# Kernel tuning notes

Measured on AMD Instinct MI355X. Metric: run time of the kernel, lower is better.

The kernel has to match this reference:

```python
import jax, jax.numpy as jnp
import numpy as np

B, S, V, D, G, H, L, K = 32, 256, 100000, 128, 128, 256, 32, 3
ALPHA = 0.5


def lstm_pass(x, mask, W, U, b, reverse):
    # x: (B,S,I), mask: (B,S) bool. PyTorch gate order i,f,g,o.
    Bh = x.shape[0]
    Hd = U.shape[0]
    h0 = jnp.zeros((Bh, Hd), x.dtype)
    c0 = jnp.zeros((Bh, Hd), x.dtype)

    def step(carry, inp):
        h, c = carry
        xt, mt = inp
        g = xt @ W + h @ U + b
        i, f, gg, o = jnp.split(g, 4, axis=-1)
        i = jax.nn.sigmoid(i)
        f = jax.nn.sigmoid(f)
        gg = jnp.tanh(gg)
        o = jax.nn.sigmoid(o)
        cn = f * c + i * gg
        hn = o * jnp.tanh(cn)
        m = mt[:, None]
        h = jnp.where(m, hn, h)
        c = jnp.where(m, cn, c)
        return (h, c), h * m.astype(h.dtype)

    _, hs = jax.lax.scan(step, (h0, c0), (x.transpose(1, 0, 2), mask.T), reverse=reverse)
    return hs.transpose(1, 0, 2)  # (B,S,Hd), zero at padded steps (like pad_packed)


def setup_inputs() -> dict:
    key = jax.random.key(0)
    ks = jax.random.split(key, 24)
    word_inputs = jax.random.randint(ks[0], (B, S), 0, V)
    lens = jnp.sort(jax.random.randint(ks[1], (B,), S // 2, S + 1))[::-1]
    mask = (jnp.arange(S)[None, :] < lens[:, None])
    idx_inputs = jax.random.randint(ks[2], (B, S), 0, V)
    char_inputs = jax.random.randint(ks[3], (B * S, 4), 0, 100)
    char_seq_lengths = jnp.ones((B * S,), jnp.int64 if jax.config.jax_enable_x64 else jnp.int32)
    char_seq_recover = jnp.arange(B * S)
    s = lambda k, sh, sc: jax.random.normal(k, sh, jnp.float32) * sc
    I = D + G
    inp = {
        'word_inputs': word_inputs,
        'word_seq_lengths': lens,
        'char_inputs': char_inputs,
        'char_seq_lengths': char_seq_lengths,
        'char_seq_recover': char_seq_recover,
        'mask': mask,
        'idx_inputs': idx_inputs,
        'word_embedding': s(ks[4], (V, D), 0.1),
        'label_embedding': s(ks[5], (L, D), 0.1),
        'sent_W': s(ks[6], (D, G), 1.0 / np.sqrt(D)),
        'sent_b': jnp.zeros((G,), jnp.float32),
        'conv_W': s(ks[7], (L, L, K), 1.0 / np.sqrt(L * K)),
        'conv_b': jnp.zeros((L,), jnp.float32),
        'lstm_Wf': s(ks[8], (I, 4 * H // 2), 1.0 / np.sqrt(I)),
        'lstm_Uf': s(ks[9], (H // 2, 4 * H // 2), 1.0 / np.sqrt(H // 2)),
        'lstm_bf': jnp.zeros((4 * H // 2,), jnp.float32),
        'lstm_Wb': s(ks[10], (I, 4 * H // 2), 1.0 / np.sqrt(I)),
        'lstm_Ub': s(ks[11], (H // 2, 4 * H // 2), 1.0 / np.sqrt(H // 2)),
        'lstm_bb': jnp.zeros((4 * H // 2,), jnp.float32),
        'tag_W': s(ks[12], (H, L), 1.0 / np.sqrt(H)),
        'tag_b': jnp.zeros((L,), jnp.float32),
        'mem_W': s(ks[13], (H, L), 1.0 / np.sqrt(H)),
        'mem_b': jnp.zeros((L,), jnp.float32),
        'mem_bank': s(ks[14], (V, H), 0.1),
    }
    return inp


def reference(word_inputs, word_seq_lengths, char_inputs, char_seq_lengths, char_seq_recover,
              mask, idx_inputs, word_embedding, label_embedding, sent_W, sent_b,
              conv_W, conv_b, lstm_Wf, lstm_Uf, lstm_bf, lstm_Wb, lstm_Ub, lstm_bb,
              tag_W, tag_b, mem_W, mem_b, mem_bank):
    maskf = mask.astype(jnp.float32)
    # ---- WordRep: embeddings + label cosine similarity ----
    we = word_embedding[word_inputs]  # (B,S,D) gather
    wn = we / (jnp.linalg.norm(we, axis=-1, keepdims=True) + 1e-8)
    ln = label_embedding / (jnp.linalg.norm(label_embedding, axis=-1, keepdims=True) + 1e-8)
    label_embs = jnp.einsum('bsd,ld->bsl', wn, ln)  # (B,S,L)
    # ---- SentenceRep (projection stand-in) + label attention pooling ----
    sent_hidden = jnp.tanh(we @ sent_W + sent_b)  # (B,S,G)
    lf = jax.lax.conv_general_dilated(
        label_embs.transpose(0, 2, 1), conv_W, (1,), [(K // 2, K // 2)],
        dimension_numbers=('NCH', 'OIH', 'NCH')) + conv_b[None, :, None]
    lf = jax.nn.relu(lf).transpose(0, 2, 1)  # (B,S,L)
    lm = lf.max(axis=-1)  # (B,S)
    # partial (masked) softmax, exactly as in the torch code
    e = jnp.exp(lm) * maskf
    attn = e / e.sum(axis=1, keepdims=True)
    sent_rep = jnp.einsum('bs,bsg->bg', attn, sent_hidden)[:, None, :]  # bmm
    sent_rep = jnp.broadcast_to(sent_rep, (B, S, G))  # repeat over seq
    # ---- BiLSTM over concat(word, sentence) ----
    wr = jnp.concatenate([we, sent_rep], axis=-1)  # (B,S,D+G)
    hf = lstm_pass(wr, mask, lstm_Wf, lstm_Uf, lstm_bf, False)
    hb = lstm_pass(wr, mask, lstm_Wb, lstm_Ub, lstm_bb, True)
    feat = jnp.concatenate([hf, hb], axis=-1)  # (B,S,H)
    outputs = feat @ tag_W + tag_b  # (B,S,L)
    # ---- MemoryBank: gather keyed by word id, zero padded positions ----
    doc_h = mem_bank[word_inputs] * maskf[..., None]  # (B,S,H) irregular gather
    doc_rep = doc_h @ mem_W + mem_b  # mem2tag
    # bank update (side effect in torch; computed functionally, not returned)
    new_bank = mem_bank.at[idx_inputs.reshape(-1)].set(
        (feat * maskf[..., None]).reshape(-1, H))
    del new_bank
    return outputs * (1.0 - ALPHA) + doc_rep * ALPHA
```

## Files before the change

### kernel.cpp

```cpp
#include <hip/hip_runtime.h>
#include <hip/hip_bf16.h>

#define BB 32
#define SS 256
#define DD 128
#define GG 128
#define NG 512
#define LL 32
#define LOG2E 1.4426950408889634f

typedef unsigned short u16;
typedef __attribute__((ext_vector_type(8))) short short8;
typedef __attribute__((ext_vector_type(4))) float f32x4;

__device__ __forceinline__ float bf2f(u16 u){ return __uint_as_float(((unsigned)u)<<16); }
__device__ __forceinline__ u16 f2bf(float f){
    unsigned x = __float_as_uint(f);
    unsigned r = x + 0x7fffu + ((x>>16)&1u);
    return (u16)(r>>16);
}
__device__ __forceinline__ float tanh_f(float x){ float e=__expf(2.0f*x); return 1.0f - 2.0f/(e+1.0f); }

__device__ __forceinline__ float exp2_f(float x){
#if __has_builtin(__builtin_amdgcn_exp2f)
    return __builtin_amdgcn_exp2f(x);
#elif __has_builtin(__builtin_amdgcn_expf)
    return __builtin_amdgcn_expf(x);
#else
    return __expf(x * 0.6931471805599453f);
#endif
}
__device__ __forceinline__ float rcp_f(float x){
#if __has_builtin(__builtin_amdgcn_rcpf)
    return __builtin_amdgcn_rcpf(x);
#else
    return 1.0f / x;
#endif
}

__global__ void kflag(const u16* __restrict__ w, int* __restrict__ flags){
    int t = threadIdx.x;
    u16 v = w[2*t];
    int e = (v>>7)&0xFF;
    __shared__ int red[256];
    red[t] = (e>=0x90)?1:0; __syncthreads();
    for (int off=128;off>0;off>>=1){ if(t<off) red[t]+=red[t+off]; __syncthreads(); }
    if (t==0) flags[0] = (red[0] >= 32) ? 1 : 0;
}

struct PJobs { const void* src[20]; int n[20]; int p0[20]; int p1[20]; int type[20]; };

__global__ void kprep(PJobs jb, const int* __restrict__ flags, float* __restrict__ can,
                      u16* __restrict__ WcatT, u16* __restrict__ tagWT, u16* __restrict__ memWT){
    int id = blockIdx.y;
    int i = blockIdx.x*256 + threadIdx.x;
    if (i >= jb.n[id]) return;
    int f = flags[0];
    const void* src = jb.src[id];
    int p0 = jb.p0[id];
    int ty = jb.type[id];
    if (ty == 0){
        float v = f ? ((const float*)src)[i] : bf2f(((const u16*)src)[i]);
        can[p0 + i] = v;
    } else if (ty == 1){
        int c = i>>7, k = i&127;
        float v = f ? ((const float*)src)[k*jb.p1[id] + c] : bf2f(((const u16*)src)[k*jb.p1[id] + c]);
        WcatT[(size_t)(p0 + c)*128 + k] = f2bf(v);
    } else {
        int l = i&31, k = i>>5;
        float v = f ? ((const float*)src)[k*32 + l] : bf2f(((const u16*)src)[k*32 + l]);
        (p0 ? memWT : tagWT)[l*256 + k] = f2bf(v);
    }
}

__global__ void k0_prep(const float* __restrict__ labc, u16* __restrict__ WcatT){
    int r = blockIdx.x, t = threadIdx.x;
    __shared__ float red[128];
    float v = labc[r*DD + t];
    red[t] = v*v; __syncthreads();
    for (int off=64; off>0; off>>=1){ if (t<off) red[t]+=red[t+off]; __syncthreads(); }
    float inv = 1.0f/(sqrtf(red[0]) + 1e-8f);
    WcatT[(size_t)(1152 + r)*128 + t] = f2bf(v*inv);
    WcatT[(size_t)(1184 + r)*128 + t] = 0;
}

__global__ void k1_token(const int* __restrict__ wid, const void* __restrict__ wemb,
                         const int* __restrict__ flags,
                         u16* __restrict__ weC, float* __restrict__ invn){
    int blk = blockIdx.x;
    int t = threadIdx.x;
    int idx = wid[blk];
    float wv = flags[0] ? ((const float*)wemb)[(size_t)idx*DD + t]
                        : bf2f(((const u16*)wemb)[(size_t)idx*DD + t]);
    int b = blk>>8, s = blk&255;
    int m = s*BB + b;
    weC[(size_t)m*DD + t] = f2bf(wv);
    float sq = wv*wv;
    #pragma unroll
    for (int mk=32; mk>0; mk>>=1) sq += __shfl_xor(sq, mk);
    __shared__ float red2[2];
    if ((t&63)==0) red2[t>>6] = sq;
    __syncthreads();
    if (t==0) invn[m] = 1.0f/(sqrtf(red2[0]+red2[1]) + 1e-8f);
}

__global__ __launch_bounds__(256) void kgemm(const u16* __restrict__ weC,
                      const u16* __restrict__ WcatT,
                      const float* __restrict__ invn, const float* __restrict__ sentBc,
                      float* __restrict__ gpre4, float* __restrict__ sent_h,
                      float* __restrict__ lab_e){
    int mt = blockIdx.x;
    int nb = blockIdx.y;
    int t = threadIdx.x;
    int w4 = t>>6, l = t&63, li = l&15, lg = l>>4;
    int mbase = mt*64 + w4*16;
    int n0 = nb*64;
    short8 af[4];
    #pragma unroll
    for (int ks=0;ks<4;ks++)
        af[ks] = *(const short8*)&weC[(size_t)(mbase + li)*128 + ks*32 + lg*8];
    f32x4 acc[4];
    #pragma unroll
    for (int nt=0;nt<4;nt++){
        short8 bf[4];
        #pragma unroll
        for (int ks=0;ks<4;ks++)
            bf[ks] = *(const short8*)&WcatT[(size_t)(n0 + nt*16 + li)*128 + ks*32 + lg*8];
        f32x4 a; a[0]=0.f; a[1]=0.f; a[2]=0.f; a[3]=0.f;
        #pragma unroll
        for (int ks=0;ks<4;ks++)
            a = __builtin_amdgcn_mfma_f32_16x16x32_bf16(af[ks], bf[ks], a, 0,0,0);
        acc[nt] = a;
    }
    int mrow = mbase + lg*4;
    #pragma unroll
    for (int nt=0;nt<4;nt++){
        int n = n0 + nt*16 + li;
        if (n < 1024){
            int dir = n>>9, n2 = n&511;
            int q = n2>>7, cc = n2&127, w5 = cc>>4, li5 = cc&15;
            float sc = (q==2) ? 2.0f*LOG2E : LOG2E;
            #pragma unroll
            for (int r=0;r<4;r++){
                int m = mrow + r;
                int b = m&31, s = m>>5;
                int bg = b>>2, rb = b&3;
                gpre4[((size_t)((dir*8+bg)*256 + s)*8 + w5)*256 + (rb*16 + li5)*4 + q] = acc[nt][r]*sc;
            }
        } else if (n < 1152){
            int c = n - 1024;
            float bb = sentBc[c];
            #pragma unroll
            for (int r=0;r<4;r++){
                int m = mrow + r;
                int b = m&31, s = m>>5;
                sent_h[((size_t)(b*256+s))*128 + c] = tanh_f(acc[nt][r] + bb);
            }
        } else if (n < 1184){
            int c = n - 1152;
            #pragma unroll
            for (int r=0;r<4;r++){
                int m = mrow + r;
                int b = m&31, s = m>>5;
                lab_e[((size_t)(b*256+s))*32 + c] = acc[nt][r] * invn[m];
            }
        }
    }
}

__global__ __launch_bounds__(256) void k2_conv(const float* __restrict__ lab_e,
                        const float* __restrict__ convWc, const float* __restrict__ convBc,
                        const int* __restrict__ lens, float* __restrict__ e_ws){
    int b = blockIdx.x, stile = blockIdx.y, t = threadIdx.x;
    int sl = t>>3, oq = t&7;
    int s = stile*32 + sl;
    __shared__ float le_s[34*33];
    __shared__ float wle[LL*LL*3];
    __shared__ float wb[LL];
    int s0 = stile*32;
    for (int i=t; i<34*32; i+=256){
        int row = i>>5, col = i&31;
        int sg = s0 - 1 + row;
        le_s[row*33 + col] = (sg>=0 && sg<SS) ? lab_e[(size_t)b*SS*LL + sg*LL + col] : 0.f;
    }
    for (int i=t; i<LL*LL*3; i+=256) wle[i] = convWc[i];
    if (t < LL) wb[t] = convBc[t];
    __syncthreads();
    float lm = 0.f;
    #pragma unroll
    for (int op=0; op<4; op++){
        int o = oq*4 + op;
        float a0 = wb[o], a1 = 0.f, a2 = 0.f;
        #pragma unroll
        for (int i=0;i<LL;i++){
            a0 = fmaf(le_s[(sl+0)*33+i], wle[o*96 + i*3    ], a0);
            a1 = fmaf(le_s[(sl+1)*33+i], wle[o*96 + i*3 + 1], a1);
            a2 = fmaf(le_s[(sl+2)*33+i], wle[o*96 + i*3 + 2], a2);
        }
        lm = fmaxf(lm, fmaxf(a0+a1+a2, 0.f));
    }
    #pragma unroll
    for (int mk=1; mk<8; mk<<=1) lm = fmaxf(lm, __shfl_xor(lm, mk));
    if (oq == 0) e_ws[b*SS + s] = (s < lens[b]) ? __expf(lm) : 0.f;
}

__global__ void k3a_attn(const float* __restrict__ e_ws, const float* __restrict__ sent_h,
                         float* __restrict__ sr){
    int b = blockIdx.x, t = threadIdx.x;
    __shared__ float es[SS], red[SS], srp[2][GG];
    float ev = e_ws[b*SS + t];
    es[t]=ev; red[t]=ev; __syncthreads();
    for (int off=128; off>0; off>>=1){ if (t<off) red[t]+=red[t+off]; __syncthreads(); }
    float inv = 1.0f/red[0];
    int col = t&127, sh = t>>7;
    float a0 = 0.f, a1 = 0.f;
    int sb = sh*128;
    for (int s2=sb; s2<sb+128; s2+=2){
        a0 = fmaf(es[s2],   sent_h[((size_t)b*SS + s2)*GG + col], a0);
        a1 = fmaf(es[s2+1], sent_h[((size_t)b*SS + s2+1)*GG + col], a1);
    }
    srp[sh][col] = a0+a1;
    __syncthreads();
    if (t < GG) sr[b*GG + t] = (srp[0][t]+srp[1][t])*inv;
}

__global__ void k3b_cpart(const float* __restrict__ sr,
                          const float* __restrict__ Wfc, const float* __restrict__ Wbc,
                          const float* __restrict__ bfc, const float* __restrict__ bbc,
                          float* __restrict__ cpart){
    int chunk = blockIdx.x, b = blockIdx.y, t = threadIdx.x;
    int ng = chunk*256 + t;
    int dir = ng>>9, n = ng&511;
    __shared__ float srs[GG];
    if (t < GG) srs[t] = sr[b*GG + t];
    __syncthreads();
    const float* W = dir ? Wbc : Wfc;
    float a0 = (dir ? bbc : bfc)[n], a1 = 0.f;
    for (int g=0; g<GG; g+=2){
        a0 = fmaf(srs[g],   W[(size_t)(DD+g)*NG + n], a0);
        a1 = fmaf(srs[g+1], W[(size_t)(DD+g+1)*NG + n], a1);
    }
    cpart[((size_t)dir*NG + n)*BB + b] = a0+a1;
}

__global__ __launch_bounds__(512) void k5_lstm(const float* __restrict__ gpre4,
                       const float* __restrict__ Ufc, const float* __restrict__ Ubc,
                       const float* __restrict__ cpart,
                       const int* __restrict__ lens, float* __restrict__ feat){
    int dir = blockIdx.x>>3, bg = blockIdx.x&7;
    int t = threadIdx.x;
    int w = t>>6, l = t&63, lg = l>>4, li = l&15;
    int j = w*16 + li;
    int b = bg*4 + lg;
    const float* Uc = dir ? Ubc : Ufc;

    short8 bfr[4][4];
    #pragma unroll
    for (int q=0;q<4;q++){
        float sc = (q==2) ? 2.0f*LOG2E : LOG2E;
        #pragma unroll
        for (int ks=0;ks<4;ks++){
            int n = q*128 + j;
            short8 v;
            #pragma unroll
            for (int jj=0;jj<8;jj++)
                v[jj] = (short)f2bf(Uc[(size_t)(ks*32 + lg*8 + jj)*NG + n] * sc);
            bfr[q][ks] = v;
        }
    }
    float cpr[4];
    #pragma unroll
    for (int q=0;q<4;q++)
        cpr[q] = cpart[((size_t)(dir*NG + q*128 + j))*BB + b] * ((q==2) ? 2.0f*LOG2E : LOG2E);
    int len1 = lens[b];

    __shared__ u16 Hhi[2][16*128];
    for (int i=t; i<2*2048; i+=512) ((u16*)Hhi)[i] = 0;

    int roff[4];
    #pragma unroll
    for (int ks=0;ks<4;ks++)
        roff[ks] = (li*256 + ((ks*64 + lg*16) ^ ((li&7)<<4))) >> 1;
    int woff;
    { int row = lg*4; woff = (row*256 + ((2*j) ^ ((row&7)<<4))) >> 1; }

    float c = 0.f, h = 0.f;
    int sgn = dir ? -1 : 1;
    int s0 = dir ? (SS-1) : 0;
    const float* gl = gpre4 + ((size_t)(dir*8 + bg)*256 + s0)*2048 + w*256 + l*4;
    ptrdiff_t gstep = (ptrdiff_t)sgn * 2048;

    f32x4 gA = *(const f32x4*)gl;
    f32x4 gB = *(const f32x4*)(gl + gstep);
    const float* glp = gl + 2*gstep;

    float* fb = feat + ((size_t)b*SS + s0)*256 + dir*128 + j;
    ptrdiff_t fstep = (ptrdiff_t)sgn * 256;

    int s = s0;
    __syncthreads();

#define K5_STEP(P, G)                                                          \
    {                                                                          \
        short8 ah[4];                                                          \
        _Pragma("unroll")                                                      \
        for (int ks=0;ks<4;ks++) ah[ks] = *(const short8*)&Hhi[P][roff[ks]];   \
        f32x4 ac[4];                                                           \
        _Pragma("unroll")                                                      \
        for (int q=0;q<4;q++){ f32x4 z; z[0]=G[q]+cpr[q]; z[1]=0.f; z[2]=0.f; z[3]=0.f; ac[q]=z; } \
        if (tt2 + 2 < SS){ G = *(const f32x4*)glp; glp += gstep; }             \
        _Pragma("unroll")                                                      \
        for (int ks=0;ks<4;ks++){                                              \
            _Pragma("unroll")                                                  \
            for (int q=0;q<4;q++)                                              \
                ac[q] = __builtin_amdgcn_mfma_f32_16x16x32_bf16(ah[ks], bfr[q][ks], ac[q], 0,0,0); \
        }                                                                      \
        float si = rcp_f(1.0f + exp2_f(-ac[0][0]));                            \
        float sf = rcp_f(1.0f + exp2_f(-ac[1][0]));                            \
        float tg = 1.0f - 2.0f*rcp_f(exp2_f(ac[2][0]) + 1.0f);                 \
        float so = rcp_f(1.0f + exp2_f(-ac[3][0]));                            \
        float cn = sf*c + si*tg;                                               \
        float th = 1.0f - 2.0f*rcp_f(exp2_f(cn*(2.0f*LOG2E)) + 1.0f);          \
        float hn = so*th;                                                      \
        if (s < 128){ c = cn; h = hn; fb[0] = hn; }                            \
        else { bool mm = (s < len1); c = mm?cn:c; h = mm?hn:h; fb[0] = mm?hn:0.f; } \
        Hhi[P^1][woff] = f2bf(h);                                              \
        asm volatile("s_waitcnt lgkmcnt(0)" ::: "memory");                     \
        __builtin_amdgcn_sched_barrier(0);                                     \
        __builtin_amdgcn_s_barrier();                                          \
        __builtin_amdgcn_sched_barrier(0);                                     \
        s += sgn; fb += fstep;                                                 \
    }

    for (int tt=0; tt<SS; tt+=2){
        { int tt2 = tt;   K5_STEP(0, gA) }
        { int tt2 = tt+1; K5_STEP(1, gB) }
    }
#undef K5_STEP
}

__global__ void k6_final(const float* __restrict__ feat, const int* __restrict__ wid,
                         const int* __restrict__ lens,
                         const u16* __restrict__ tagWT, const float* __restrict__ tagBc,
                         const u16* __restrict__ memWT, const float* __restrict__ memBc,
                         const void* __restrict__ bank, const int* __restrict__ flags,
                         void* __restrict__ out){
    int t = threadIdx.x;
    int tok = blockIdx.x*8 + (t>>5);
    int lcol = t&31;
    int b = tok>>8, s = tok&255;
    int f32m = flags[0];
    int idx = wid[tok];
    bool m = s < lens[b];
    const float* fr = feat + (size_t)tok*256;
    float a0 = tagBc[lcol], a1=0.f, a2=0.f, a3=0.f;
    #pragma unroll 4
    for (int cc=0; cc<32; cc++){
        short8 tw = *(const short8*)&tagWT[lcol*256 + cc*8];
        a0 = fmaf(fr[cc*8+0], bf2f((u16)tw[0]), a0);
        a1 = fmaf(fr[cc*8+1], bf2f((u16)tw[1]), a1);
        a2 = fmaf(fr[cc*8+2], bf2f((u16)tw[2]), a2);
        a3 = fmaf(fr[cc*8+3], bf2f((u16)tw[3]), a3);
        a0 = fmaf(fr[cc*8+4], bf2f((u16)tw[4]), a0);
        a1 = fmaf(fr[cc*8+5], bf2f((u16)tw[5]), a1);
        a2 = fmaf(fr[cc*8+6], bf2f((u16)tw[6]), a2);
        a3 = fmaf(fr[cc*8+7], bf2f((u16)tw[7]), a3);
    }
    float r1 = (a0+a1)+(a2+a3);
    float b0 = memBc[lcol], b1=0.f, b2=0.f, b3=0.f;
    if (m){
        if (f32m){
            const float* br = (const float*)bank + (size_t)idx*256;
            #pragma unroll 4
            for (int cc=0; cc<32; cc++){
                short8 tw = *(const short8*)&memWT[lcol*256 + cc*8];
                b0 = fmaf(br[cc*8+0], bf2f((u16)tw[0]), b0);
                b1 = fmaf(br[cc*8+1], bf2f((u16)tw[1]), b1);
                b2 = fmaf(br[cc*8+2], bf2f((u16)tw[2]), b2);
                b3 = fmaf(br[cc*8+3], bf2f((u16)tw[3]), b3);
                b0 = fmaf(br[cc*8+4], bf2f((u16)tw[4]), b0);
                b1 = fmaf(br[cc*8+5], bf2f((u16)tw[5]), b1);
                b2 = fmaf(br[cc*8+6], bf2f((u16)tw[6]), b2);
                b3 = fmaf(br[cc*8+7], bf2f((u16)tw[7]), b3);
            }
        } else {
            const u16* br = (const u16*)bank + (size_t)idx*256;
            #pragma unroll 4
            for (int cc=0; cc<32; cc++){
                short8 tw = *(const short8*)&memWT[lcol*256 + cc*8];
                short8 bv = *(const short8*)&br[cc*8];
                b0 = fmaf(bf2f((u16)bv[0]), bf2f((u16)tw[0]), b0);
                b1 = fmaf(bf2f((u16)bv[1]), bf2f((u16)tw[1]), b1);
                b2 = fmaf(bf2f((u16)bv[2]), bf2f((u16)tw[2]), b2);
                b3 = fmaf(bf2f((u16)bv[3]), bf2f((u16)tw[3]), b3);
                b0 = fmaf(bf2f((u16)bv[4]), bf2f((u16)tw[4]), b0);
                b1 = fmaf(bf2f((u16)bv[5]), bf2f((u16)tw[5]), b1);
                b2 = fmaf(bf2f((u16)bv[6]), bf2f((u16)tw[6]), b2);
                b3 = fmaf(bf2f((u16)bv[7]), bf2f((u16)tw[7]), b3);
            }
        }
    }
    float r2 = (b0+b1)+(b2+b3);
    float res = 0.5f*r1 + 0.5f*r2;
    if (f32m) ((float*)out)[(size_t)tok*LL + lcol] = res;
    else      ((u16*)out)[(size_t)tok*LL + lcol]   = f2bf(res);
}

extern "C" void kernel_launch(void* const* d_in, const int* in_sizes, int n_in,
                              void* d_out, int out_size, void* d_ws, size_t ws_size,
                              hipStream_t stream){
    const int* wid  = (const int*)d_in[0];
    const int* lens = (const int*)d_in[1];

    char* ws = (char*)d_ws;
    int*   flags  = (int*)  (ws + 0);
    float* can    = (float*)(ws + 1024);
    u16*   WcatT  = (u16*)  (ws + 1900544);
    u16*   tagWT  = (u16*)  (ws + 2211840);
    u16*   memWT  = (u16*)  (ws + 2228224);
    float* invn   = (float*)(ws + 2244608);
    float* cpart  = (float*)(ws + 2277376);
    float* e_ws   = (float*)(ws + 2408448);
    float* sr     = (float*)(ws + 2441216);
    u16*   weC    = (u16*)  (ws + 4194304);
    float* lab_e  = (float*)(ws + 8388608);
    float* sent_h = (float*)(ws + 9437184);
    float* gpre4  = (float*)(ws + 16777216);
    float* feat   = (float*)(ws + 50331648);

    float* labc   = can + 0;
    float* sentBc = can + 20480;
    float* convWc = can + 20608;
    float* convBc = can + 23680;
    float* Wfc    = can + 23712;
    float* Wbc    = can + 154784;
    float* bfc    = can + 285856;
    float* bbc    = can + 286368;
    float* Ufc    = can + 286880;
    float* Ubc    = can + 352416;
    float* tagBc  = can + 426144;
    float* memBc  = can + 434368;

    static const int cn_n[15]   = {4096,16384,128,3072,32,131072,131072,512,512,65536,65536,8192,32,8192,32};
    static const int cn_src[15] = {8,9,10,11,12,13,16,15,18,14,17,19,20,21,22};
    PJobs jb;
    {
        int off = 0;
        for (int i=0;i<15;i++){
            jb.src[i]=d_in[cn_src[i]]; jb.n[i]=cn_n[i]; jb.p0[i]=off; jb.p1[i]=0; jb.type[i]=0;
            off+=cn_n[i];
        }
        jb.src[15]=d_in[13]; jb.n[15]=65536; jb.p0[15]=0;    jb.p1[15]=512; jb.type[15]=1;
        jb.src[16]=d_in[16]; jb.n[16]=65536; jb.p0[16]=512;  jb.p1[16]=512; jb.type[16]=1;
        jb.src[17]=d_in[9];  jb.n[17]=16384; jb.p0[17]=1024; jb.p1[17]=128; jb.type[17]=1;
        jb.src[18]=d_in[19]; jb.n[18]=8192;  jb.p0[18]=0;    jb.p1[18]=0;   jb.type[18]=2;
        jb.src[19]=d_in[21]; jb.n[19]=8192;  jb.p0[19]=1;    jb.p1[19]=0;   jb.type[19]=2;
    }

    kflag  <<<1, 256, 0, stream>>>((const u16*)d_in[7], flags);
    kprep  <<<dim3(512,20), 256, 0, stream>>>(jb, flags, can, WcatT, tagWT, memWT);
    k0_prep<<<32, 128, 0, stream>>>(labc, WcatT);
    k1_token<<<8192, 128, 0, stream>>>(wid, d_in[7], flags, weC, invn);
    kgemm  <<<dim3(128,19), 256, 0, stream>>>(weC, WcatT, invn, sentBc, gpre4, sent_h, lab_e);
    k2_conv<<<dim3(32,8), 256, 0, stream>>>(lab_e, convWc, convBc, lens, e_ws);
    k3a_attn<<<32, 256, 0, stream>>>(e_ws, sent_h, sr);
    k3b_cpart<<<dim3(4,32), 256, 0, stream>>>(sr, Wfc, Wbc, bfc, bbc, cpart);
    k5_lstm<<<16, 512, 0, stream>>>(gpre4, Ufc, Ubc, cpart, lens, feat);
    k6_final<<<1024, 256, 0, stream>>>(feat, wid, lens, tagWT, tagBc, memWT, memBc,
                                       d_in[23], flags, d_out);
}
```

Measured before the change: 246.9 us.

## Fold flag detection and label norm into kprep, fuse attention with cpart, split LSTM MFMA chains

Removes three small launches by computing the dtype flag inside every kprep block, handling label-embedding normalization as a new kprep job type, and merging the attention reduction with the cpart projection in one kernel. In the LSTM recurrence it splits the four-deep MFMA accumulation into two independent chains to shorten dependency latency. It also masks LDS reads of h so only lanes with li%4==0 load, and adds an occupancy hint to launch_bounds. The fused k3 kernel now runs the cpart work on only 32 blocks instead of 128, and the masked h reads zero out most of the MFMA input rows.

Result: slower. 363.8 us (+47.3%).

```diff
diff --git a/kernel.cpp b/kernel.cpp
--- a/kernel.cpp
+++ b/kernel.cpp
@@ -38,24 +38,31 @@
 #endif
 }
 
-__global__ void kflag(const u16* __restrict__ w, int* __restrict__ flags){
+struct PJobs { const void* src[21]; int n[21]; int p0[21]; int p1[21]; int type[21]; };
+
+__global__ void kprep(PJobs jb, const void* __restrict__ wemb, int* __restrict__ flags,
+                      float* __restrict__ can,
+                      u16* __restrict__ WcatT, u16* __restrict__ tagWT, u16* __restrict__ memWT){
     int t = threadIdx.x;
-    u16 v = w[2*t];
-    int e = (v>>7)&0xFF;
-    __shared__ int red[256];
-    red[t] = (e>=0x90)?1:0; __syncthreads();
-    for (int off=128;off>0;off>>=1){ if(t<off) red[t]+=red[t+off]; __syncthreads(); }
-    if (t==0) flags[0] = (red[0] >= 32) ? 1 : 0;
-}
-
-struct PJobs { const void* src[20]; int n[20]; int p0[20]; int p1[20]; int type[20]; };
-
-__global__ void kprep(PJobs jb, const int* __restrict__ flags, float* __restrict__ can,
-                      u16* __restrict__ WcatT, u16* __restrict__ tagWT, u16* __restrict__ memWT){
+    __shared__ int cw[4];
+    __shared__ int sflag;
+    {
+        u16 v = ((const u16*)wemb)[2*t];
+        int e = (v>>7)&0xFF;
+        int c = (e>=0x90)?1:0;
+        #pragma unroll
+        for (int mk=32; mk>0; mk>>=1) c += __shfl_xor(c, mk);
+        if ((t&63)==0) cw[t>>6] = c;
+        __syncthreads();
+        if (t==0) sflag = (cw[0]+cw[1]+cw[2]+cw[3] >= 32) ? 1 : 0;
+        __syncthreads();
+    }
+    int f = sflag;
+    if (blockIdx.x==0 && blockIdx.y==0 && t==0) flags[0] = f;
+
     int id = blockIdx.y;
-    int i = blockIdx.x*256 + threadIdx.x;
+    int i = blockIdx.x*256 + t;
     if (i >= jb.n[id]) return;
-    int f = flags[0];
     const void* src = jb.src[id];
     int p0 = jb.p0[id];
     int ty = jb.type[id];
@@ -66,22 +73,25 @@
         int c = i>>7, k = i&127;
         float v = f ? ((const float*)src)[k*jb.p1[id] + c] : bf2f(((const u16*)src)[k*jb.p1[id] + c]);
         WcatT[(size_t)(p0 + c)*128 + k] = f2bf(v);
-    } else {
+    } else if (ty == 2){
         int l = i&31, k = i>>5;
         float v = f ? ((const float*)src)[k*32 + l] : bf2f(((const u16*)src)[k*32 + l]);
         (p0 ? memWT : tagWT)[l*256 + k] = f2bf(v);
-    }
-}
-
-__global__ void k0_prep(const float* __restrict__ labc, u16* __restrict__ WcatT){
-    int r = blockIdx.x, t = threadIdx.x;
-    __shared__ float red[128];
-    float v = labc[r*DD + t];
-    red[t] = v*v; __syncthreads();
-    for (int off=64; off>0; off>>=1){ if (t<off) red[t]+=red[t+off]; __syncthreads(); }
-    float inv = 1.0f/(sqrtf(red[0]) + 1e-8f);
-    WcatT[(size_t)(1152 + r)*128 + t] = f2bf(v*inv);
-    WcatT[(size_t)(1184 + r)*128 + t] = 0;
+    } else {
+        int row = i>>7, col = i&127;
+        float v = f ? ((const float*)src)[i] : bf2f(((const u16*)src)[i]);
+        float sq = v*v;
+        #pragma unroll
+        for (int mk=32; mk>0; mk>>=1) sq += __shfl_xor(sq, mk);
+        __shared__ float r4[4];
+        if ((t&63)==0) r4[t>>6] = sq;
+        __syncthreads();
+        int half = t>>7;
+        float tot = r4[half*2] + r4[half*2+1];
+        float inv = 1.0f/(sqrtf(tot) + 1e-8f);
+        WcatT[(size_t)(1152+row)*128 + col] = f2bf(v*inv);
+        WcatT[(size_t)(1184+row)*128 + col] = 0;
+    }
 }
 
 __global__ void k1_token(const int* __restrict__ wid, const void* __restrict__ wemb,
@@ -204,10 +214,12 @@
     if (oq == 0) e_ws[b*SS + s] = (s < lens[b]) ? __expf(lm) : 0.f;
 }
 
-__global__ void k3a_attn(const float* __restrict__ e_ws, const float* __restrict__ sent_h,
-                         float* __restrict__ sr){
+__global__ void k3_attn(const float* __restrict__ e_ws, const float* __restrict__ sent_h,
+                        const float* __restrict__ Wfc, const float* __restrict__ Wbc,
+                        const float* __restrict__ bfc, const float* __restrict__ bbc,
+                        float* __restrict__ cpart){
     int b = blockIdx.x, t = threadIdx.x;
-    __shared__ float es[SS], red[SS], srp[2][GG];
+    __shared__ float es[SS], red[SS], srp[2][GG], srs[GG];
     float ev = e_ws[b*SS + t];
     es[t]=ev; red[t]=ev; __syncthreads();
     for (int off=128; off>0; off>>=1){ if (t<off) red[t]+=red[t+off]; __syncthreads(); }
@@ -221,29 +233,23 @@
     }
     srp[sh][col] = a0+a1;
     __syncthreads();
-    if (t < GG) sr[b*GG + t] = (srp[0][t]+srp[1][t])*inv;
-}
-
-__global__ void k3b_cpart(const float* __restrict__ sr,
-                          const float* __restrict__ Wfc, const float* __restrict__ Wbc,
-                          const float* __restrict__ bfc, const float* __restrict__ bbc,
-                          float* __restrict__ cpart){
-    int chunk = blockIdx.x, b = blockIdx.y, t = threadIdx.x;
-    int ng = chunk*256 + t;
-    int dir = ng>>9, n = ng&511;
-    __shared__ float srs[GG];
-    if (t < GG) srs[t] = sr[b*GG + t];
+    if (t < GG) srs[t] = (srp[0][t]+srp[1][t])*inv;
     __syncthreads();
-    const float* W = dir ? Wbc : Wfc;
-    float a0 = (dir ? bbc : bfc)[n], a1 = 0.f;
-    for (int g=0; g<GG; g+=2){
-        a0 = fmaf(srs[g],   W[(size_t)(DD+g)*NG + n], a0);
-        a1 = fmaf(srs[g+1], W[(size_t)(DD+g+1)*NG + n], a1);
-    }
-    cpart[((size_t)dir*NG + n)*BB + b] = a0+a1;
-}
-
-__global__ __launch_bounds__(512) void k5_lstm(const float* __restrict__ gpre4,
+    #pragma unroll
+    for (int chunk=0; chunk<4; chunk++){
+        int ng = chunk*256 + t;
+        int dir = ng>>9, n = ng&511;
+        const float* W = dir ? Wbc : Wfc;
+        float c0 = (dir ? bbc : bfc)[n], c1 = 0.f;
+        for (int g=0; g<GG; g+=2){
+            c0 = fmaf(srs[g],   W[(size_t)(DD+g)*NG + n], c0);
+            c1 = fmaf(srs[g+1], W[(size_t)(DD+g+1)*NG + n], c1);
+        }
+        cpart[((size_t)dir*NG + n)*BB + b] = c0+c1;
+    }
+}
+
+__global__ __launch_bounds__(512,2) void k5_lstm(const float* __restrict__ gpre4,
                        const float* __restrict__ Ufc, const float* __restrict__ Ubc,
                        const float* __restrict__ cpart,
                        const int* __restrict__ lens, float* __restrict__ feat){
@@ -277,6 +283,7 @@
     __shared__ u16 Hhi[2][16*128];
     for (int i=t; i<2*2048; i+=512) ((u16*)Hhi)[i] = 0;
 
+    bool rdp = ((li & 3) == 0);
     int roff[4];
     #pragma unroll
     for (int ks=0;ks<4;ks++)
@@ -304,21 +311,35 @@
     {                                                                          \
         short8 ah[4];                                                          \
         _Pragma("unroll")                                                      \
-        for (int ks=0;ks<4;ks++) ah[ks] = *(const short8*)&Hhi[P][roff[ks]];   \
-        f32x4 ac[4];                                                           \
+        for (int ks=0;ks<4;ks++){                                              \
+            short8 a;                                                          \
+            _Pragma("unroll")                                                  \
+            for (int jj=0;jj<8;jj++) a[jj] = 0;                                \
+            if (rdp) a = *(const short8*)&Hhi[P][roff[ks]];                    \
+            ah[ks] = a;                                                        \
+        }                                                                      \
+        f32x4 acA[4], acB[4];                                                  \
         _Pragma("unroll")                                                      \
-        for (int q=0;q<4;q++){ f32x4 z; z[0]=G[q]+cpr[q]; z[1]=0.f; z[2]=0.f; z[3]=0.f; ac[q]=z; } \
+        for (int q=0;q<4;q++){                                                 \
+            f32x4 z; z[0]=G[q]+cpr[q]; z[1]=0.f; z[2]=0.f; z[3]=0.f; acA[q]=z; \
+            f32x4 z2; z2[0]=0.f; z2[1]=0.f; z2[2]=0.f; z2[3]=0.f; acB[q]=z2;   \
+        }                                                                      \
         if (tt2 + 2 < SS){ G = *(const f32x4*)glp; glp += gstep; }             \
         _Pragma("unroll")                                                      \
-        for (int ks=0;ks<4;ks++){                                              \
-            _Pragma("unroll")                                                  \
-            for (int q=0;q<4;q++)                                              \
-                ac[q] = __builtin_amdgcn_mfma_f32_16x16x32_bf16(ah[ks], bfr[q][ks], ac[q], 0,0,0); \
+        for (int q=0;q<4;q++){                                                 \
+            acA[q] = __builtin_amdgcn_mfma_f32_16x16x32_bf16(ah[0], bfr[q][0], acA[q], 0,0,0); \
+            acB[q] = __builtin_amdgcn_mfma_f32_16x16x32_bf16(ah[2], bfr[q][2], acB[q], 0,0,0); \
+            acA[q] = __builtin_amdgcn_mfma_f32_16x16x32_bf16(ah[1], bfr[q][1], acA[q], 0,0,0); \
+            acB[q] = __builtin_amdgcn_mfma_f32_16x16x32_bf16(ah[3], bfr[q][3], acB[q], 0,0,0); \
         }                                                                      \
-        float si = rcp_f(1.0f + exp2_f(-ac[0][0]));                            \
-        float sf = rcp_f(1.0f + exp2_f(-ac[1][0]));                            \
-        float tg = 1.0f - 2.0f*rcp_f(exp2_f(ac[2][0]) + 1.0f);                 \
-        float so = rcp_f(1.0f + exp2_f(-ac[3][0]));                            \
+        float xg0 = acA[0][0] + acB[0][0];                                     \
+        float xg1 = acA[1][0] + acB[1][0];                                     \
+        float xg2 = acA[2][0] + acB[2][0];                                     \
+        float xg3 = acA[3][0] + acB[3][0];                                     \
+        float si = rcp_f(1.0f + exp2_f(-xg0));                                 \
+        float sf = rcp_f(1.0f + exp2_f(-xg1));                                 \
+        float tg = 1.0f - 2.0f*rcp_f(exp2_f(xg2) + 1.0f);                      \
+        float so = rcp_f(1.0f + exp2_f(-xg3));                                 \
         float cn = sf*c + si*tg;                                               \
         float th = 1.0f - 2.0f*rcp_f(exp2_f(cn*(2.0f*LOG2E)) + 1.0f);          \
         float hn = so*th;                                                      \
@@ -421,14 +442,12 @@
     float* invn   = (float*)(ws + 2244608);
     float* cpart  = (float*)(ws + 2277376);
     float* e_ws   = (float*)(ws + 2408448);
-    float* sr     = (float*)(ws + 2441216);
     u16*   weC    = (u16*)  (ws + 4194304);
     float* lab_e  = (float*)(ws + 8388608);
     float* sent_h = (float*)(ws + 9437184);
     float* gpre4  = (float*)(ws + 16777216);
     float* feat   = (float*)(ws + 50331648);
 
-    float* labc   = can + 0;
     float* sentBc = can + 20480;
     float* convWc = can + 20608;
     float* convBc = can + 23680;
@@ -455,16 +474,14 @@
         jb.src[17]=d_in[9];  jb.n[17]=16384; jb.p0[17]=1024; jb.p1[17]=128; jb.type[17]=1;
         jb.src[18]=d_in[19]; jb.n[18]=8192;  jb.p0[18]=0;    jb.p1[18]=0;   jb.type[18]=2;
         jb.src[19]=d_in[21]; jb.n[19]=8192;  jb.p0[19]=1;    jb.p1[19]=0;   jb.type[19]=2;
-    }
-
-    kflag  <<<1, 256, 0, stream>>>((const u16*)d_in[7], flags);
-    kprep  <<<dim3(512,20), 256, 0, stream>>>(jb, flags, can, WcatT, tagWT, memWT);
-    k0_prep<<<32, 128, 0, stream>>>(labc, WcatT);
+        jb.src[20]=d_in[8];  jb.n[20]=4096;  jb.p0[20]=0;    jb.p1[20]=0;   jb.type[20]=3;
+    }
+
+    kprep  <<<dim3(512,21), 256, 0, stream>>>(jb, d_in[7], flags, can, WcatT, tagWT, memWT);
     k1_token<<<8192, 128, 0, stream>>>(wid, d_in[7], flags, weC, invn);
     kgemm  <<<dim3(128,19), 256, 0, stream>>>(weC, WcatT, invn, sentBc, gpre4, sent_h, lab_e);
     k2_conv<<<dim3(32,8), 256, 0, stream>>>(lab_e, convWc, convBc, lens, e_ws);
-    k3a_attn<<<32, 256, 0, stream>>>(e_ws, sent_h, sr);
-    k3b_cpart<<<dim3(4,32), 256, 0, stream>>>(sr, Wfc, Wbc, bfc, bbc, cpart);
+    k3_attn<<<32, 256, 0, stream>>>(e_ws, sent_h, Wfc, Wbc, bfc, bbc, cpart);
     k5_lstm<<<16, 512, 0, stream>>>(gpre4, Ufc, Ubc, cpart, lens, feat);
     k6_final<<<1024, 256, 0, stream>>>(feat, wid, lens, tagWT, tagBc, memWT, memBc,
                                        d_in[23], flags, d_out);
```
